# Optimization experiments

Hardware: AMD Instinct MI355X
Metric: run time of the kernel (lower is better)

## Reference

```python
import jax, jax.numpy as jnp
import numpy as np

N = 20000      # nodes
E = 320000     # edges
F = 128        # feat_dim
N_RBF = 20
CUTOFF = 5.0


def setup_inputs() -> dict:
    key = jax.random.key(0)
    ks = jax.random.split(key, 12)
    h_i = jax.random.normal(ks[0], (N, F), dtype=jnp.float32)
    v_i = jax.random.normal(ks[1], (N, F, 3), dtype=jnp.float32)
    # distances in (0, cutoff); keep strictly > 0 to avoid div-by-zero in sinc basis
    d_ij = (jax.random.uniform(ks[2], (E,), dtype=jnp.float32) * 0.98 + 0.01) * CUTOFF
    r = jax.random.normal(ks[3], (E, 3), dtype=jnp.float32)
    unit_r_ij = r / jnp.linalg.norm(r, axis=-1, keepdims=True)
    nbrs = jax.random.randint(ks[4], (E, 2), 0, N, dtype=jnp.int64)
    # params: layers = Dense(F->F, swish) then Dense(F->3F); dist_embed dense: n_rbf -> 3F
    s1 = 1.0 / np.sqrt(F)
    W1 = jax.random.uniform(ks[5], (F, F), jnp.float32, -s1, s1)
    b1 = jax.random.uniform(ks[6], (F,), jnp.float32, -s1, s1)
    W2 = jax.random.uniform(ks[7], (F, 3 * F), jnp.float32, -s1, s1)
    b2 = jax.random.uniform(ks[8], (3 * F,), jnp.float32, -s1, s1)
    sr = 1.0 / np.sqrt(N_RBF)
    Wr = jax.random.uniform(ks[9], (N_RBF, 3 * F), jnp.float32, -sr, sr)
    br = jax.random.uniform(ks[10], (3 * F,), jnp.float32, -sr, sr)
    return {"h_i": h_i, "v_i": v_i, "d_ij": d_ij, "unit_r_ij": unit_r_ij,
            "nbrs": nbrs, "W1": W1, "b1": b1, "W2": W2, "b2": b2, "Wr": Wr, "br": br}


def _dist_embed(d, Wr, br):
    # PaiNN sinc-like radial basis: sin(n*pi*d/cutoff)/d, n=1..N_RBF
    n = jnp.arange(1, N_RBF + 1, dtype=d.dtype)
    rbf = jnp.sin(n[None, :] * jnp.pi * d[:, None] / CUTOFF) / d[:, None]  # [E, N_RBF]
    # cosine cutoff envelope
    fcut = 0.5 * (jnp.cos(jnp.pi * d / CUTOFF) + 1.0) * (d < CUTOFF)       # [E]
    return (rbf @ Wr + br) * fcut[:, None]                                  # [E, 3F]


def reference(h_i, v_i, d_ij, unit_r_ij, nbrs, W1, b1, W2, b2, Wr, br):
    # phi = Dense(swish) -> Dense : [N, 3F]
    phi = jax.nn.silu(h_i @ W1 + b1) @ W2 + b2
    src = nbrs[:, 1]
    dst = nbrs[:, 0]
    edge_inv = phi[src] * _dist_embed(d_ij, Wr, br)          # [E, 3F]
    edge_inv = edge_inv.reshape(edge_inv.shape[0], 3, F)     # [E, 3, F]
    f1, f2, f3 = edge_inv[:, 0], edge_inv[:, 1], edge_inv[:, 2]
    # dv: [E, F, 3]
    dv = f1[:, :, None] * unit_r_ij[:, None, :] + f2[:, :, None] * v_i[src]
    dh_i = jax.ops.segment_sum(f3, dst, num_segments=N)      # [N, F]
    dv_i = jax.ops.segment_sum(dv, dst, num_segments=N)      # [N, F, 3]
    return (dh_i, dv_i)
```

## Files before the change

### kernel.cpp

```cpp
#include <hip/hip_runtime.h>
#include <math.h>

#define F 128
#define THREEF 384
#define N_RBF 20
#define CUTOFF 5.0f
#define CAP 64
#define TLDS_STRIDE 136

typedef __bf16 bf16x8 __attribute__((ext_vector_type(8)));
typedef float  f32x4  __attribute__((ext_vector_type(4)));

__global__ __launch_bounds__(256) void prep_kernel(
    const float* __restrict__ d_ij, const float* __restrict__ unit_r,
    const int* __restrict__ nbrs,
    const float* __restrict__ W1, const float* __restrict__ W2,
    const float* __restrict__ Wr,
    int* __restrict__ cnt, float* __restrict__ pack,
    __bf16* __restrict__ W1T, __bf16* __restrict__ W2T,
    float* __restrict__ WrT, int E, int EB)
{
    const int tid = threadIdx.x;
    const int b   = blockIdx.x;

    if (b < EB) {
        const int e = b * 256 + tid;
        if (e >= E) return;
        const int2 nb = ((const int2*)nbrs)[e];
        const int dst = nb.x;
        const int src = nb.y;
        const int slot = atomicAdd(&cnt[dst], 1);
        if (slot >= CAP) return;

        const float d = d_ij[e];
        const float x = (float)M_PI * d * (1.0f / CUTOFF);
        float sx, cx;
        __sincosf(x, &sx, &cx);
        const float fcut = (d < CUTOFF) ? 0.5f * (cx + 1.0f) : 0.0f;
        float4 q0, q1;
        q0.x = sx * fcut / d;
        q0.y = 2.0f * cx;
        q0.z = fcut;
        q0.w = unit_r[3 * e + 0];
        q1.x = unit_r[3 * e + 1];
        q1.y = unit_r[3 * e + 2];
        q1.z = __int_as_float(src);
        q1.w = 0.0f;
        float4* pk = (float4*)(pack + ((size_t)dst * CAP + slot) * 8);
        pk[0] = q0;
        pk[1] = q1;
    } else if (b < EB + 256) {
        const int idx = (b - EB) * 256 + tid;
        if (idx < 128 * 128) {
            const int n = idx >> 7, k = idx & 127;
            W1T[idx] = (__bf16)W1[k * F + n];
        }
        if (idx < 384 * 128) {
            const int n = idx >> 7, k = idx & 127;
            W2T[idx] = (__bf16)W2[k * THREEF + n];
        }
    } else {
        const int idx = (b - EB - 256) * 256 + tid;
        if (idx >= 5 * 3 * 128) return;
        const int f  = idx & 127;
        const int c  = (idx >> 7) % 3;
        const int n4 = idx / (3 * 128);
        float4 v;
        v.x = Wr[(4 * n4 + 0) * THREEF + c * 128 + f];
        v.y = Wr[(4 * n4 + 1) * THREEF + c * 128 + f];
        v.z = Wr[(4 * n4 + 2) * THREEF + c * 128 + f];
        v.w = Wr[(4 * n4 + 3) * THREEF + c * 128 + f];
        ((float4*)WrT)[idx] = v;
    }
}

__global__ __launch_bounds__(256) void mlp_mfma_kernel(
    const float* __restrict__ h,
    const __bf16* __restrict__ W1T,
    const float* __restrict__ b1,
    const __bf16* __restrict__ W2T,
    const float* __restrict__ b2,
    float* __restrict__ phi, int N)
{
    __shared__ __bf16 t_lds[4][16 * TLDS_STRIDE];

    const int wave = threadIdx.x >> 6;
    const int lane = threadIdx.x & 63;
    const int m    = lane & 15;
    const int quad = lane >> 4;
    const int node0 = blockIdx.x * 64 + wave * 16;
    if (node0 >= N) return;

    bf16x8 a1[4];
    #pragma unroll
    for (int kb = 0; kb < 4; ++kb) {
        const float* hp = h + (size_t)(node0 + m) * F + kb * 32 + quad * 8;
        const float4 x0 = *(const float4*)hp;
        const float4 x1 = *(const float4*)(hp + 4);
        bf16x8 a;
        a[0] = (__bf16)x0.x; a[1] = (__bf16)x0.y;
        a[2] = (__bf16)x0.z; a[3] = (__bf16)x0.w;
        a[4] = (__bf16)x1.x; a[5] = (__bf16)x1.y;
        a[6] = (__bf16)x1.z; a[7] = (__bf16)x1.w;
        a1[kb] = a;
    }

    #pragma unroll
    for (int ct = 0; ct < 8; ++ct) {
        f32x4 acc = {0.0f, 0.0f, 0.0f, 0.0f};
        #pragma unroll
        for (int kb = 0; kb < 4; ++kb) {
            const bf16x8 b =
                *(const bf16x8*)(W1T + (size_t)(ct * 16 + m) * F + kb * 32 + quad * 8);
            acc = __builtin_amdgcn_mfma_f32_16x16x32_bf16(a1[kb], b, acc, 0, 0, 0);
        }
        const int col = ct * 16 + m;
        const float bb = b1[col];
        #pragma unroll
        for (int reg = 0; reg < 4; ++reg) {
            const float x = acc[reg] + bb;
            const float s = x / (1.0f + __expf(-x));
            t_lds[wave][(quad * 4 + reg) * TLDS_STRIDE + col] = (__bf16)s;
        }
    }

    bf16x8 a2[4];
    #pragma unroll
    for (int kb = 0; kb < 4; ++kb)
        a2[kb] = *(const bf16x8*)&t_lds[wave][m * TLDS_STRIDE + kb * 32 + quad * 8];

    #pragma unroll
    for (int ct = 0; ct < 24; ++ct) {
        f32x4 acc = {0.0f, 0.0f, 0.0f, 0.0f};
        #pragma unroll
        for (int kb = 0; kb < 4; ++kb) {
            const bf16x8 b =
                *(const bf16x8*)(W2T + (size_t)(ct * 16 + m) * F + kb * 32 + quad * 8);
            acc = __builtin_amdgcn_mfma_f32_16x16x32_bf16(a2[kb], b, acc, 0, 0, 0);
        }
        const int col   = ct * 16 + m;
        const int plane = col >> 7;
        const int fc    = col & 127;
        const float bb  = b2[col];
        #pragma unroll
        for (int reg = 0; reg < 4; ++reg) {
            const int row = quad * 4 + reg;
            phi[((((size_t)(node0 + row)) * F + fc) << 2) + plane] = acc[reg] + bb;
        }
    }
}

__global__ __launch_bounds__(256, 4) void gather_kernel(
    const float4* __restrict__ phi4,
    const float* __restrict__ v_i,
    const float* __restrict__ WrT,
    const float* __restrict__ br,
    const int*   __restrict__ cnt,
    const float* __restrict__ pack,
    float* __restrict__ dh,
    float* __restrict__ dv,
    int N)
{
    __shared__ float4 s_pack[2][CAP * 2];
    __shared__ float  s_rbf[2][CAP * 20];

    const int tid  = threadIdx.x;
    const int half = tid >> 7;
    const int f    = tid & 127;
    const int node = blockIdx.x * 2 + half;

    const int deg0 = cnt[node];
    const int deg  = deg0 < CAP ? deg0 : CAP;

    {
        const float4* src = (const float4*)(pack + (size_t)node * CAP * 8);
        if (f < 2 * deg) s_pack[half][f] = src[f];
    }

    const float4* wTg = (const float4*)WrT;
    float w[60];
    #pragma unroll
    for (int j = 0; j < 15; ++j) {
        const float4 t = wTg[j * 128 + f];
        w[4 * j + 0] = t.x; w[4 * j + 1] = t.y;
        w[4 * j + 2] = t.z; w[4 * j + 3] = t.w;
    }
    #pragma unroll
    for (int j = 0; j < 60; ++j) asm volatile("" : "+v"(w[j]));

    __syncthreads();

    if (f < deg) {
        const float* q = (const float*)&s_pack[half][2 * f];
        float rp = 0.0f, rc = q[0];
        const float twoc = q[1];
        float* rb = &s_rbf[half][f * 20];
        rb[0] = rc;
        #pragma unroll
        for (int n = 1; n < 20; ++n) {
            const float rn = fmaf(twoc, rc, -rp);
            rp = rc; rc = rn;
            rb[n] = rc;
        }
    }
    __syncthreads();

    const float br0 = br[f], br1 = br[f + 128], br2 = br[f + 256];

    float dh_acc = 0.0f, dv0 = 0.0f, dv1 = 0.0f, dv2 = 0.0f;

    for (int i = 0; i < deg; ++i) {
        const float* q = (const float*)&s_pack[half][2 * i];
        const float fcut = q[2];
        const float ux   = q[3];
        const float uy   = q[4];
        const float uz   = q[5];
        const int src = __builtin_amdgcn_readfirstlane(__float_as_int(q[6]));

        const float* rb = &s_rbf[half][i * 20];

        float a0 = br0 * fcut, a1 = br1 * fcut, a2 = br2 * fcut;
        #pragma unroll
        for (int n4 = 0; n4 < 5; ++n4) {
            #pragma unroll
            for (int k = 0; k < 4; ++k) {
                const float rn = rb[n4 * 4 + k];
                a0 = fmaf(rn, w[(n4 * 3 + 0) * 4 + k], a0);
                a1 = fmaf(rn, w[(n4 * 3 + 1) * 4 + k], a1);
                a2 = fmaf(rn, w[(n4 * 3 + 2) * 4 + k], a2);
            }
        }

        const float4 ph = phi4[(size_t)src * F + f];
        const float f1 = ph.x * a0;
        const float f2 = ph.y * a1;
        const float f3 = ph.z * a2;

        dh_acc += f3;

        const float* vs = v_i + (size_t)src * THREEF + 3 * f;
        dv0 = fmaf(f1, ux, fmaf(f2, vs[0], dv0));
        dv1 = fmaf(f1, uy, fmaf(f2, vs[1], dv1));
        dv2 = fmaf(f1, uz, fmaf(f2, vs[2], dv2));
    }

    dh[(size_t)node * F + f] = dh_acc;
    float* dvp = dv + (size_t)node * THREEF + 3 * f;
    dvp[0] = dv0;
    dvp[1] = dv1;
    dvp[2] = dv2;
}

extern "C" void kernel_launch(void* const* d_in, const int* in_sizes, int n_in,
                              void* d_out, int out_size, void* d_ws, size_t ws_size,
                              hipStream_t stream) {
    const float* h_i    = (const float*)d_in[0];
    const float* v_i    = (const float*)d_in[1];
    const float* d_ij   = (const float*)d_in[2];
    const float* unit_r = (const float*)d_in[3];
    const int*   nbrs   = (const int*)  d_in[4];
    const float* W1     = (const float*)d_in[5];
    const float* b1     = (const float*)d_in[6];
    const float* W2     = (const float*)d_in[7];
    const float* b2     = (const float*)d_in[8];
    const float* Wr     = (const float*)d_in[9];
    const float* br     = (const float*)d_in[10];

    const int N = in_sizes[0] / F;
    const int E = in_sizes[2];

    float* dh = (float*)d_out;
    float* dv = dh + (size_t)N * F;

    float*  phi  = (float*)d_ws;
    float*  pack = phi + (size_t)4 * N * F;
    float*  WrT  = pack + (size_t)N * CAP * 8;
    int*    cnt  = (int*)(WrT + 5 * 3 * 128 * 4);
    __bf16* W1T  = (__bf16*)(cnt + N);
    __bf16* W2T  = W1T + 128 * 128;

    const int EB = (E + 255) / 256;

    hipMemsetAsync(cnt, 0, (size_t)N * sizeof(int), stream);

    prep_kernel<<<EB + 256 + 8, 256, 0, stream>>>(
        d_ij, unit_r, nbrs, W1, W2, Wr, cnt, pack, W1T, W2T, WrT, E, EB);
    mlp_mfma_kernel<<<(N + 63) / 64, 256, 0, stream>>>(h_i, W1T, b1, W2T, b2,
                                                       phi, N);
    gather_kernel<<<N / 2, 256, 0, stream>>>((const float4*)phi, v_i, WrT, br,
                                             cnt, pack, dh, dv, N);
}
```

Baseline: 318.6 us.

## Stage RBF weights in LDS and process edges four at a time

Moves the per-thread 60-register copy of the transposed RBF weights into a shared LDS array loaded cooperatively by the block. The edge loop is unrolled by four, with degree padded to a multiple of four using zeroed pack entries, so four phi and v_i gathers are issued before their use. The weight move is meant to free registers and raise occupancy, and the batching is meant to hide gather latency. In exchange it costs 30KB of LDS per block, which may limit occupancy, adds LDS weight reads per batch, and does wasted work on padded edges.

```diff
diff --git a/kernel.cpp b/kernel.cpp
--- a/kernel.cpp
+++ b/kernel.cpp
@@ -161,6 +161,7 @@
     float* __restrict__ dv,
     int N)
 {
+    __shared__ float4 sw[15 * 128];
     __shared__ float4 s_pack[2][CAP * 2];
     __shared__ float  s_rbf[2][CAP * 20];
 
@@ -169,28 +170,24 @@
     const int f    = tid & 127;
     const int node = blockIdx.x * 2 + half;
 
+    const float4* wTg = (const float4*)WrT;
+    for (int idx = tid; idx < 15 * 128; idx += 256) sw[idx] = wTg[idx];
+
     const int deg0 = cnt[node];
     const int deg  = deg0 < CAP ? deg0 : CAP;
+    const int degR = (deg + 3) & ~3;
 
     {
-        const float4* src = (const float4*)(pack + (size_t)node * CAP * 8);
-        if (f < 2 * deg) s_pack[half][f] = src[f];
-    }
-
-    const float4* wTg = (const float4*)WrT;
-    float w[60];
-    #pragma unroll
-    for (int j = 0; j < 15; ++j) {
-        const float4 t = wTg[j * 128 + f];
-        w[4 * j + 0] = t.x; w[4 * j + 1] = t.y;
-        w[4 * j + 2] = t.z; w[4 * j + 3] = t.w;
-    }
-    #pragma unroll
-    for (int j = 0; j < 60; ++j) asm volatile("" : "+v"(w[j]));
-
+        const float4* srcp = (const float4*)(pack + (size_t)node * CAP * 8);
+        if (f < 2 * degR) {
+            float4 v = make_float4(0.0f, 0.0f, 0.0f, 0.0f);
+            if (f < 2 * deg) v = srcp[f];
+            s_pack[half][f] = v;
+        }
+    }
     __syncthreads();
 
-    if (f < deg) {
+    if (f < degR) {
         const float* q = (const float*)&s_pack[half][2 * f];
         float rp = 0.0f, rc = q[0];
         const float twoc = q[1];
@@ -209,39 +206,63 @@
 
     float dh_acc = 0.0f, dv0 = 0.0f, dv1 = 0.0f, dv2 = 0.0f;
 
-    for (int i = 0; i < deg; ++i) {
-        const float* q = (const float*)&s_pack[half][2 * i];
-        const float fcut = q[2];
-        const float ux   = q[3];
-        const float uy   = q[4];
-        const float uz   = q[5];
-        const int src = __builtin_amdgcn_readfirstlane(__float_as_int(q[6]));
-
-        const float* rb = &s_rbf[half][i * 20];
-
-        float a0 = br0 * fcut, a1 = br1 * fcut, a2 = br2 * fcut;
+    for (int i0 = 0; i0 < degR; i0 += 4) {
+        float fcut[4], ux[4], uy[4], uz[4];
+        float4 ph[4];
+        float vx[4], vy[4], vz[4];
+
+        #pragma unroll
+        for (int j = 0; j < 4; ++j) {
+            const float* q = (const float*)&s_pack[half][2 * (i0 + j)];
+            fcut[j] = q[2]; ux[j] = q[3]; uy[j] = q[4]; uz[j] = q[5];
+            const int src = __builtin_amdgcn_readfirstlane(__float_as_int(q[6]));
+            ph[j] = phi4[(size_t)src * F + f];
+            const float* vs = v_i + (size_t)src * THREEF + 3 * f;
+            vx[j] = vs[0]; vy[j] = vs[1]; vz[j] = vs[2];
+        }
+
+        float a0[4], a1[4], a2[4];
+        #pragma unroll
+        for (int j = 0; j < 4; ++j) {
+            a0[j] = br0 * fcut[j];
+            a1[j] = br1 * fcut[j];
+            a2[j] = br2 * fcut[j];
+        }
+
         #pragma unroll
         for (int n4 = 0; n4 < 5; ++n4) {
+            const float4 w0 = sw[(n4 * 3 + 0) * 128 + f];
+            const float4 w1 = sw[(n4 * 3 + 1) * 128 + f];
+            const float4 w2 = sw[(n4 * 3 + 2) * 128 + f];
             #pragma unroll
-            for (int k = 0; k < 4; ++k) {
-                const float rn = rb[n4 * 4 + k];
-                a0 = fmaf(rn, w[(n4 * 3 + 0) * 4 + k], a0);
-                a1 = fmaf(rn, w[(n4 * 3 + 1) * 4 + k], a1);
-                a2 = fmaf(rn, w[(n4 * 3 + 2) * 4 + k], a2);
+            for (int j = 0; j < 4; ++j) {
+                const float4 rb =
+                    *(const float4*)&s_rbf[half][(i0 + j) * 20 + n4 * 4];
+                a0[j] = fmaf(rb.x, w0.x, a0[j]);
+                a1[j] = fmaf(rb.x, w1.x, a1[j]);
+                a2[j] = fmaf(rb.x, w2.x, a2[j]);
+                a0[j] = fmaf(rb.y, w0.y, a0[j]);
+                a1[j] = fmaf(rb.y, w1.y, a1[j]);
+                a2[j] = fmaf(rb.y, w2.y, a2[j]);
+                a0[j] = fmaf(rb.z, w0.z, a0[j]);
+                a1[j] = fmaf(rb.z, w1.z, a1[j]);
+                a2[j] = fmaf(rb.z, w2.z, a2[j]);
+                a0[j] = fmaf(rb.w, w0.w, a0[j]);
+                a1[j] = fmaf(rb.w, w1.w, a1[j]);
+                a2[j] = fmaf(rb.w, w2.w, a2[j]);
             }
         }
 
-        const float4 ph = phi4[(size_t)src * F + f];
-        const float f1 = ph.x * a0;
-        const float f2 = ph.y * a1;
-        const float f3 = ph.z * a2;
-
-        dh_acc += f3;
-
-        const float* vs = v_i + (size_t)src * THREEF + 3 * f;
-        dv0 = fmaf(f1, ux, fmaf(f2, vs[0], dv0));
-        dv1 = fmaf(f1, uy, fmaf(f2, vs[1], dv1));
-        dv2 = fmaf(f1, uz, fmaf(f2, vs[2], dv2));
+        #pragma unroll
+        for (int j = 0; j < 4; ++j) {
+            const float f1 = ph[j].x * a0[j];
+            const float f2 = ph[j].y * a1[j];
+            const float f3 = ph[j].z * a2[j];
+            dh_acc += f3;
+            dv0 = fmaf(f1, ux[j], fmaf(f2, vx[j], dv0));
+            dv1 = fmaf(f1, uy[j], fmaf(f2, vy[j], dv1));
+            dv2 = fmaf(f1, uz[j], fmaf(f2, vz[j], dv2));
+        }
     }
 
     dh[(size_t)node * F + f] = dh_acc;
```

Measured after the change: 342.4 us. 7.5% more time.
